# Performance work log

Hardware: AMD Instinct MI355X
Metric: run time of the kernel (lower is better)

Reference implementation:

```python
import jax, jax.numpy as jnp
import numpy as np

R_CUTOFF = 5.0
BASIS = 8
NMAX = 8
NSPECIES = 3
EMBED = 16


def _chebyshev_basis(r, r_cutoff, basis_size):
    fc = jnp.where(r < r_cutoff, 0.5 * jnp.cos(jnp.pi * r / r_cutoff) + 0.5, 0.0)
    x = 2.0 * (r / r_cutoff) ** 2 - 1.0
    polys = [jnp.ones_like(x), x]
    for n in range(2, basis_size):
        polys.append(2.0 * x * polys[-1] - polys[-2])
    basis = jnp.stack(polys[:basis_size], axis=-1)  # [E, basis]
    return 0.5 * (basis + 1.0) * fc[:, None]


def setup_inputs() -> dict:
    key = jax.random.key(0)
    ks = jax.random.split(key, 12)
    N, K = 20000, 32
    E = N * K
    positions = jax.random.normal(ks[0], (N, 3), dtype=jnp.float32)
    species = jax.random.randint(ks[1], (N,), 0, NSPECIES, dtype=jnp.int32)
    magmoms = jax.random.normal(ks[2], (N, 3), dtype=jnp.float32)
    # i-major edge list: exactly K edges per atom, grouped by center atom.
    i_idx = jnp.repeat(jnp.arange(N, dtype=jnp.int32), K)
    j_idx = jax.random.randint(ks[3], (E,), 0, N, dtype=jnp.int32)
    edge_index = jnp.stack([i_idx, j_idx], axis=0)
    shifts = jnp.zeros((E, 3), dtype=jnp.float32)
    rb_coefficients = 0.1 * jax.random.normal(ks[4], (NSPECIES * NSPECIES, NMAX, BASIS), dtype=jnp.float32)
    species_embedding = 0.1 * jax.random.normal(ks[5], (NSPECIES, EMBED), dtype=jnp.float32)
    struct_dim = NMAX + NMAX * (NMAX + 1)  # 80
    mag_dim = 3 + 7 * NMAX + 3 * NMAX * NMAX  # 251
    return {
        'positions': positions, 'species': species, 'magmoms': magmoms,
        'edge_index': edge_index, 'shifts': shifts,
        'rb_coefficients': rb_coefficients, 'species_embedding': species_embedding,
        'struct_shift': jnp.zeros(struct_dim, jnp.float32),
        'struct_scale': jnp.ones(struct_dim, jnp.float32),
        'mag_shift': jnp.zeros(mag_dim, jnp.float32),
        'mag_scale': jnp.ones(mag_dim, jnp.float32),
        'atomic_energy_shift': 0.1 * jax.random.normal(ks[6], (NSPECIES,), dtype=jnp.float32),
        'w_struct': 0.05 * jax.random.normal(ks[7], (EMBED + struct_dim,), dtype=jnp.float32),
        'b_struct': 0.05 * jax.random.normal(ks[8], (1,), dtype=jnp.float32),
        'w_mag': 0.05 * jax.random.normal(ks[9], (EMBED + mag_dim,), dtype=jnp.float32),
        'b_mag': 0.05 * jax.random.normal(ks[10], (1,), dtype=jnp.float32),
    }


def _forward(positions, magmoms, shifts, rb_coefficients, species_embedding,
             struct_shift, struct_scale, mag_shift, mag_scale, atomic_energy_shift,
             w_struct, b_struct, w_mag, b_mag, species, edge_index):
    N = positions.shape[0]
    E = edge_index.shape[1]
    K = E // N  # regular neighbor count (edge list is i-major)
    i_idx, j_idx = edge_index[0], edge_index[1]
    r_ij = positions[j_idx] - positions[i_idx] + shifts          # [E,3]
    dist = jnp.linalg.norm(r_ij, axis=-1)                        # [E]
    f_k = _chebyshev_basis(dist, R_CUTOFF, BASIS)                # [E,basis]
    pair_idx = species[i_idx] * NSPECIES + species[j_idx]
    phi = jnp.einsum('enk,ek->en', rb_coefficients[pair_idx], f_k)  # [E,n]
    seg = lambda x: jax.ops.segment_sum(x, i_idx, num_segments=N)
    d = jnp.maximum(dist, 1e-8)[:, None]
    r_hat = r_ij / d
    # --- structural descriptors ---
    d_radial = seg(phi)                                          # [N,n]
    P = seg(phi[:, :, None] * r_hat[:, None, :])                 # [N,n,3]
    PP = jnp.einsum('ina,ima->inm', P, P)
    tu = np.triu_indices(NMAX)
    d_ang_l1 = PP[:, tu[0], tu[1]]
    eye3 = jnp.eye(3, dtype=r_ij.dtype)
    traceless = r_hat[:, :, None] * r_hat[:, None, :] - eye3 / 3.0  # [E,3,3]
    Q = seg(phi[:, :, None, None] * traceless[:, None, :, :])       # [N,n,3,3]
    Qf = Q.reshape(N, NMAX, 9)
    QQ = jnp.einsum('ina,ima->inm', Qf, Qf)
    d_ang_l2 = QQ[:, tu[0], tu[1]]
    desc_struct = jnp.concatenate([d_radial, d_ang_l1, d_ang_l2], axis=-1)
    # --- magnetic descriptors ---
    u = jnp.sum(magmoms * magmoms, axis=-1)                      # [N]
    m_norm = jnp.linalg.norm(magmoms, axis=-1, keepdims=True)
    m_dir = jnp.where(m_norm > 1e-8, magmoms / jnp.maximum(m_norm, 1e-8), 0.0)
    M = seg(phi[:, :, None] * m_dir[j_idx][:, None, :])          # [N,n,3]
    # A_{nm}(i) = sum_{a<b within atom i's edge block} phi_n(a) phi_m(b) (r_a x r_b)
    phi_g = phi.reshape(N, K, NMAX)
    r_g = r_ij.reshape(N, K, 3)
    cross = jnp.cross(r_g[:, :, None, :], r_g[:, None, :, :])    # [N,K,K,3]
    mask = jnp.triu(jnp.ones((K, K), dtype=phi.dtype), k=1)
    tmp = jnp.einsum('iabd,ab,ibm->iamd', cross, mask, phi_g)    # [N,K,3,n]
    A = jnp.einsum('ian,iamd->inmd', phi_g, tmp)                 # [N,n,n,3]
    d_amp = jnp.stack([u, u ** 2, u ** 3], axis=-1)
    d_iso = jnp.sum(m_dir[:, None, :] * M, axis=-1)              # [N,n]
    Qm = jnp.einsum('anij,aj->ani', Q, m_dir)
    d_sia = jnp.sum(m_dir[:, None, :] * Qm, axis=-1)
    mQ = jnp.einsum('ai,amij->amj', m_dir, Q)
    d_sae = jnp.einsum('amj,anj->amn', mQ, M).reshape(N, -1)
    m_cross_M = jnp.cross(jnp.broadcast_to(m_dir[:, None, :], M.shape), M)
    d_dmi = jnp.einsum('inmd,imd->inm', A, m_cross_M).reshape(N, -1)
    u_col = u[:, None]
    d_amp_mix = jnp.concatenate([u_col * d_iso, u_col * d_sia, u_col * d_dmi], axis=-1)
    u_j = u[j_idx]
    d_nbr_amp = seg(phi * u_j[:, None])
    W = seg(phi[:, :, None] * (u_j[:, None] * m_dir[j_idx])[:, None, :])
    d_nbr_amp_ex = jnp.sum(m_dir[:, None, :] * W, axis=-1)
    d_nbr_amp_ex_mix = u_col * d_nbr_amp_ex
    desc_mag = jnp.concatenate([d_amp, d_iso, d_sia, d_sae, d_dmi, d_amp_mix,
                                d_nbr_amp, d_nbr_amp_ex, d_nbr_amp_ex_mix], axis=-1)
    # --- scaling + linear readout heads + per-species shift ---
    ds = (desc_struct - struct_shift) / struct_scale
    dm = (desc_mag - mag_shift) / mag_scale
    emb = species_embedding[species]
    e_struct = jnp.concatenate([emb, ds], axis=-1) @ w_struct + b_struct[0]
    e_mag = jnp.concatenate([emb, dm], axis=-1) @ w_mag + b_mag[0]
    return e_struct + e_mag + atomic_energy_shift[species]        # [N]


def reference(positions, species, magmoms, edge_index, shifts, rb_coefficients,
              species_embedding, struct_shift, struct_scale, mag_shift, mag_scale,
              atomic_energy_shift, w_struct, b_struct, w_mag, b_mag):
    return _forward(positions, magmoms, shifts, rb_coefficients, species_embedding,
                    struct_shift, struct_scale, mag_shift, mag_scale, atomic_energy_shift,
                    w_struct, b_struct, w_mag, b_mag, species, edge_index)
```

## Files before the change

kernel.cpp:

```cpp
#include <hip/hip_runtime.h>

#define NSPEC  3
#define EMBEDD 16
#define KMAX   32
#define RCUT   5.0f
#define PADR   36

__constant__ int TUN[36] = {0,0,0,0,0,0,0,0, 1,1,1,1,1,1,1, 2,2,2,2,2,2, 3,3,3,3,3, 4,4,4,4, 5,5,5, 6,6, 7};
__constant__ int TUM[36] = {0,1,2,3,4,5,6,7, 1,2,3,4,5,6,7, 2,3,4,5,6,7, 3,4,5,6,7, 4,5,6,7, 5,6,7, 6,7, 7};


template<int CTRL, int RMASK, bool BC>
__device__ __forceinline__ float dpp_mov0(float x) {
    return __int_as_float(__builtin_amdgcn_update_dpp(
        0, __float_as_int(x), CTRL, RMASK, 0xF, BC));
}
__device__ __forceinline__ float prefix32(float x) {
    x += dpp_mov0<0x111, 0xF, true >(x);
    x += dpp_mov0<0x112, 0xF, true >(x);
    x += dpp_mov0<0x114, 0xF, true >(x);
    x += dpp_mov0<0x118, 0xF, true >(x);
    x += dpp_mov0<0x142, 0xA, false>(x);
    return x;
}
__device__ __forceinline__ float swz_xor16(float x) {
    return __int_as_float(__builtin_amdgcn_ds_swizzle(__float_as_int(x), 0x401F));
}
__device__ __forceinline__ float red_k4(float x) {
    x += dpp_mov0<0x128, 0xF, true>(x);
    x += swz_xor16(x);
    return x;
}
__device__ __forceinline__ float red32(float x) {
    x += dpp_mov0<0x121, 0xF, true>(x);
    x += dpp_mov0<0x122, 0xF, true>(x);
    x += dpp_mov0<0x124, 0xF, true>(x);
    x += dpp_mov0<0x128, 0xF, true>(x);
    x += swz_xor16(x);
    return x;
}

__device__ __forceinline__ void lds_fence() {
    asm volatile("s_waitcnt lgkmcnt(0)" ::: "memory");
}

struct __align__(16) AtomLds {
    float phiT[8 * PADR];
    float rhx[KMAX], rhy[KMAX], rhz[KMAX];
    float mdx[KMAX], mdy[KMAX], mdz[KMAX];
    float uj[KMAX];
    float P4[8*4];
    float Q8[8*8];
    float M4[8*4];
    float mQ4[8*4];
    float wv4[8*4];
};

__global__ __launch_bounds__(256)
void magpot_setup(const float* __restrict__ sshift, const float* __restrict__ sscale,
                  const float* __restrict__ mshift, const float* __restrict__ mscale,
                  const float* __restrict__ wstruct, const float* __restrict__ bstruct,
                  const float* __restrict__ wmag, const float* __restrict__ bmag,
                  float* __restrict__ ws)
{
    __shared__ float red[4];
    const int t = threadIdx.x;
    float c = 0.0f;
    for (int idx = t; idx < 80; idx += 256) {
        const float w = wstruct[16 + idx] / sscale[idx];
        ws[idx] = w;
        c += w * sshift[idx];
    }
    for (int idx = t; idx < 251; idx += 256) {
        const float w = wmag[16 + idx] / mscale[idx];
        ws[80 + idx] = w;
        c += w * mshift[idx];
    }
    if (t < EMBEDD) ws[332 + t] = wstruct[t] + wmag[t];
    if (t < 64) {
        const int n = t >> 3, m = t & 7;
        ws[400 + m*8 + n] = wmag[16 + 83 + t]  / mscale[83 + t];
        ws[464 + m*8 + n] = wmag[16 + 163 + t] / mscale[163 + t];
    }
    #pragma unroll
    for (int d = 1; d <= 32; d <<= 1) c += __shfl_xor(c, d, 64);
    if ((t & 63) == 0) red[t >> 6] = c;
    __syncthreads();
    if (t == 0) ws[331] = bstruct[0] + bmag[0] - (red[0] + red[1] + red[2] + red[3]);
}

__global__ __launch_bounds__(256)
void magpot_main(const float* __restrict__ pos,
                 const int*   __restrict__ species,
                 const float* __restrict__ mag,
                 const int*   __restrict__ eidx,
                 const float* __restrict__ shifts,
                 const float* __restrict__ rb,
                 const float* __restrict__ semb,
                 const float* __restrict__ aes,
                 const float* __restrict__ ws,
                 float* __restrict__ out,
                 int N, int E, int K)
{
    __shared__ AtomLds lds[8];

    const int lane64 = threadIdx.x & 63;
    const int wv     = threadIdx.x >> 6;
    const int h      = lane64 >> 5;
    const int s      = lane64 & 31;
    const int ea     = 31 - s;
    const int i      = blockIdx.x * 8 + wv * 2 + h;
    const bool valid = (i < N);
    const int isafe  = valid ? i : 0;
    AtomLds& L = lds[wv * 2 + h];

    const float* wm = ws + 80;

    const float pix = pos[3*isafe+0], piy = pos[3*isafe+1], piz = pos[3*isafe+2];
    const int   spi = species[isafe];
    const float mgx = mag[3*isafe+0], mgy = mag[3*isafe+1], mgz = mag[3*isafe+2];
    const float u_i = mgx*mgx + mgy*mgy + mgz*mgz;
    const float mn_i = sqrtf(u_i);
    const float mi_inv = (mn_i > 1e-8f) ? (1.0f / mn_i) : 0.0f;
    const float mix = mgx*mi_inv, miy = mgy*mi_inv, miz = mgz*mi_inv;

    float phi[8];
    float rx = 0.0f, ry = 0.0f, rz = 0.0f;
    #pragma unroll
    for (int n = 0; n < 8; ++n) phi[n] = 0.0f;

    if (ea < K) {
        const int e = isafe * K + ea;
        const int j = eidx[E + e];
        rx = pos[3*j+0] - pix + shifts[3*e+0];
        ry = pos[3*j+1] - piy + shifts[3*e+1];
        rz = pos[3*j+2] - piz + shifts[3*e+2];
        const float dist = sqrtf(rx*rx + ry*ry + rz*rz);
        const float fc = (dist < RCUT)
            ? (0.5f * __builtin_amdgcn_cosf(dist * 0.1f) + 0.5f)
            : 0.0f;
        const float xr = dist * (1.0f/RCUT);
        const float x  = 2.0f * xr * xr - 1.0f;
        float f[8];
        {
            float Tm2 = 1.0f, Tm1 = x;
            f[0] = 0.5f * (Tm2 + 1.0f) * fc;
            f[1] = 0.5f * (Tm1 + 1.0f) * fc;
            #pragma unroll
            for (int k = 2; k < 8; ++k) {
                const float T = 2.0f * x * Tm1 - Tm2;
                Tm2 = Tm1; Tm1 = T;
                f[k] = 0.5f * (T + 1.0f) * fc;
            }
        }
        const int spj = species[j];
        const float4* rb4 = (const float4*)(rb + (spi * NSPEC + spj) * 64);
        #pragma unroll
        for (int n = 0; n < 8; ++n) {
            const float4 r0 = rb4[n*2+0];
            const float4 r1 = rb4[n*2+1];
            const float ph = r0.x*f[0] + r0.y*f[1] + r0.z*f[2] + r0.w*f[3]
                           + r1.x*f[4] + r1.y*f[5] + r1.z*f[6] + r1.w*f[7];
            phi[n] = ph;
            L.phiT[n*PADR + ea] = ph;
        }
        const float dinv = 1.0f / fmaxf(dist, 1e-8f);
        L.rhx[ea] = rx * dinv;
        L.rhy[ea] = ry * dinv;
        L.rhz[ea] = rz * dinv;
        const float mjx = mag[3*j+0], mjy = mag[3*j+1], mjz = mag[3*j+2];
        const float uj = mjx*mjx + mjy*mjy + mjz*mjz;
        const float mnj = sqrtf(uj);
        const float mjinv = (mnj > 1e-8f) ? (1.0f / mnj) : 0.0f;
        L.mdx[ea] = mjx * mjinv;
        L.mdy[ea] = mjy * mjinv;
        L.mdz[ea] = mjz * mjinv;
        L.uj[ea] = uj;
    } else {
        #pragma unroll
        for (int n = 0; n < 8; ++n) L.phiT[n*PADR + ea] = 0.0f;
        L.rhx[ea] = 0.0f; L.rhy[ea] = 0.0f; L.rhz[ea] = 0.0f;
        L.mdx[ea] = 0.0f; L.mdy[ea] = 0.0f; L.mdz[ea] = 0.0f;
        L.uj[ea] = 0.0f;
    }
    lds_fence();

    float p = 0.0f;

    {
        const int k4 = s >> 3;
        const int n  = s & 7;
        const float4* phR = (const float4*)&L.phiT[n*PADR + k4*8];
        const float4* hxR = (const float4*)&L.rhx[k4*8];
        const float4* hyR = (const float4*)&L.rhy[k4*8];
        const float4* hzR = (const float4*)&L.rhz[k4*8];
        const float4* dxR = (const float4*)&L.mdx[k4*8];
        const float4* dyR = (const float4*)&L.mdy[k4*8];
        const float4* dzR = (const float4*)&L.mdz[k4*8];
        const float4* ujR = (const float4*)&L.uj[k4*8];

        float a_dr = 0.0f;
        float aP0 = 0.0f, aP1 = 0.0f, aP2 = 0.0f;
        float aQ0 = 0.0f, aQ1 = 0.0f, aQ2 = 0.0f, aQ3 = 0.0f, aQ4 = 0.0f, aQ5 = 0.0f;
        float aM0 = 0.0f, aM1 = 0.0f, aM2 = 0.0f;
        float a_nb = 0.0f;
        float aW0 = 0.0f, aW1 = 0.0f, aW2 = 0.0f;

        auto acc = [&](float ph, float hx, float hy, float hz,
                       float dx, float dy, float dz, float uj) {
            a_dr += ph;
            aP0 += ph*hx; aP1 += ph*hy; aP2 += ph*hz;
            aQ0 += ph*(hx*hx - (1.0f/3.0f));
            aQ1 += ph*(hx*hy);
            aQ2 += ph*(hx*hz);
            aQ3 += ph*(hy*hy - (1.0f/3.0f));
            aQ4 += ph*(hy*hz);
            aQ5 += ph*(hz*hz - (1.0f/3.0f));
            aM0 += ph*dx; aM1 += ph*dy; aM2 += ph*dz;
            const float pu = ph*uj;
            a_nb += pu;
            aW0 += pu*dx; aW1 += pu*dy; aW2 += pu*dz;
        };
        #pragma unroll
        for (int q = 0; q < 2; ++q) {
            const float4 ph4 = phR[q], hx4 = hxR[q], hy4 = hyR[q], hz4 = hzR[q];
            const float4 dx4 = dxR[q], dy4 = dyR[q], dz4 = dzR[q], uj4 = ujR[q];
            acc(ph4.x, hx4.x, hy4.x, hz4.x, dx4.x, dy4.x, dz4.x, uj4.x);
            acc(ph4.y, hx4.y, hy4.y, hz4.y, dx4.y, dy4.y, dz4.y, uj4.y);
            acc(ph4.z, hx4.z, hy4.z, hz4.z, dx4.z, dy4.z, dz4.z, uj4.z);
            acc(ph4.w, hx4.w, hy4.w, hz4.w, dx4.w, dy4.w, dz4.w, uj4.w);
        }
        a_dr = red_k4(a_dr);
        aP0 = red_k4(aP0); aP1 = red_k4(aP1); aP2 = red_k4(aP2);
        aQ0 = red_k4(aQ0); aQ1 = red_k4(aQ1); aQ2 = red_k4(aQ2);
        aQ3 = red_k4(aQ3); aQ4 = red_k4(aQ4); aQ5 = red_k4(aQ5);
        aM0 = red_k4(aM0); aM1 = red_k4(aM1); aM2 = red_k4(aM2);
        a_nb = red_k4(a_nb);
        aW0 = red_k4(aW0); aW1 = red_k4(aW1); aW2 = red_k4(aW2);

        if (k4 == 0) {
            ((float4*)L.P4)[n]      = make_float4(aP0, aP1, aP2, 0.0f);
            ((float4*)L.Q8)[2*n]    = make_float4(aQ0, aQ1, aQ2, aQ3);
            ((float4*)L.Q8)[2*n+1]  = make_float4(aQ4, aQ5, 0.0f, 0.0f);
            ((float4*)L.M4)[n]      = make_float4(aM0, aM1, aM2, 0.0f);
            const float mq0 = aQ0*mix + aQ1*miy + aQ2*miz;
            const float mq1 = aQ1*mix + aQ3*miy + aQ4*miz;
            const float mq2 = aQ2*mix + aQ4*miy + aQ5*miz;
            ((float4*)L.mQ4)[n]     = make_float4(mq0, mq1, mq2, 0.0f);
            ((float4*)L.wv4)[n]     = make_float4(miy*aM2 - miz*aM1,
                                                  miz*aM0 - mix*aM2,
                                                  mix*aM1 - miy*aM0, 0.0f);
            const float diso = mix*aM0 + miy*aM1 + miz*aM2;
            const float dsia = aQ0*mix*mix + aQ3*miy*miy + aQ5*miz*miz
                             + 2.0f*(aQ1*mix*miy + aQ2*mix*miz + aQ4*miy*miz);
            const float dnex = mix*aW0 + miy*aW1 + miz*aW2;
            p += a_dr * ws[n] + a_nb * wm[227 + n]
               + diso * wm[3 + n]  + dsia * wm[11 + n]  + dnex * wm[235 + n]
               + u_i * (diso * wm[147 + n] + dsia * wm[155 + n] + dnex * wm[243 + n]);
        }
        if (s == 8) {
            const float u2 = u_i * u_i;
            p += u_i * wm[0] + u2 * wm[1] + u2 * u_i * wm[2];
        }
        if (s < EMBEDD)
            p += semb[spi * EMBEDD + s] * ws[332 + s];
    }
    lds_fence();

    {
        float B[8];
        #pragma unroll
        for (int m = 0; m < 8; ++m) {
            float a1 = 0.0f, a2 = 0.0f;
            #pragma unroll
            for (int n = 0; n < 8; ++n) {
                a1 = fmaf(phi[n], ws[400 + m*8 + n], a1);
                a2 = fmaf(phi[n], ws[464 + m*8 + n], a2);
            }
            B[m] = a1 + u_i * a2;
        }
        float cdmi = 0.0f;
        #pragma unroll
        for (int m = 0; m < 8; ++m) {
            const float4 wvm = ((const float4*)L.wv4)[m];
            const float vx = phi[m] * rx;
            const float vy = phi[m] * ry;
            const float vz = phi[m] * rz;
            const float Sx = prefix32(vx) - vx;
            const float Sy = prefix32(vy) - vy;
            const float Sz = prefix32(vz) - vz;
            const float cx = ry*Sz - rz*Sy;
            const float cy = rz*Sx - rx*Sz;
            const float cz = rx*Sy - ry*Sx;
            cdmi = fmaf(B[m], cx*wvm.x + cy*wvm.y + cz*wvm.z, cdmi);
        }
        p += cdmi;
    }

    {
        #pragma unroll
        for (int t2 = 0; t2 < 2; ++t2) {
            const int idx = s + t2*32;
            const int m4 = idx >> 3, n4 = idx & 7;
            const float4 mQm = ((const float4*)L.mQ4)[m4];
            const float4 Mn  = ((const float4*)L.M4)[n4];
            p += (mQm.x*Mn.x + mQm.y*Mn.y + mQm.z*Mn.z) * wm[19 + idx];
        }
        #pragma unroll
        for (int t2 = 0; t2 < 2; ++t2) {
            const int idx = s + t2*32;
            if (idx < 36) {
                const int a = TUN[idx], b = TUM[idx];
                const float4 Pa = ((const float4*)L.P4)[a];
                const float4 Pb = ((const float4*)L.P4)[b];
                const float pp = Pa.x*Pb.x + Pa.y*Pb.y + Pa.z*Pb.z;
                const float4 Qa0 = ((const float4*)L.Q8)[2*a], Qa1 = ((const float4*)L.Q8)[2*a+1];
                const float4 Qb0 = ((const float4*)L.Q8)[2*b], Qb1 = ((const float4*)L.Q8)[2*b+1];
                const float qq = Qa0.x*Qb0.x + Qa0.w*Qb0.w + Qa1.y*Qb1.y
                       + 2.0f*(Qa0.y*Qb0.y + Qa0.z*Qb0.z + Qa1.x*Qb1.x);
                p += pp * ws[8 + idx] + qq * ws[44 + idx];
            }
        }
    }

    p = red32(p);
    if (s == 0 && valid)
        out[i] = p + ws[331] + aes[spi];
}

extern "C" void kernel_launch(void* const* d_in, const int* in_sizes, int n_in,
                              void* d_out, int out_size, void* d_ws, size_t ws_size,
                              hipStream_t stream) {
    const float* pos     = (const float*)d_in[0];
    const int*   spc     = (const int*)  d_in[1];
    const float* mg      = (const float*)d_in[2];
    const int*   eidx    = (const int*)  d_in[3];
    const float* shf     = (const float*)d_in[4];
    const float* rb      = (const float*)d_in[5];
    const float* semb    = (const float*)d_in[6];
    const float* sshift  = (const float*)d_in[7];
    const float* sscale  = (const float*)d_in[8];
    const float* mshift  = (const float*)d_in[9];
    const float* mscale  = (const float*)d_in[10];
    const float* aes     = (const float*)d_in[11];
    const float* wstruct = (const float*)d_in[12];
    const float* bstruct = (const float*)d_in[13];
    const float* wmag    = (const float*)d_in[14];
    const float* bmag    = (const float*)d_in[15];
    float* out = (float*)d_out;
    float* ws  = (float*)d_ws;

    const int N = in_sizes[1];
    const int E = in_sizes[3] / 2;
    const int K = E / N;

    hipLaunchKernelGGL(magpot_setup, dim3(1), dim3(256), 0, stream,
                       sshift, sscale, mshift, mscale, wstruct, bstruct, wmag, bmag, ws);
    hipLaunchKernelGGL(magpot_main, dim3((N + 7) / 8), dim3(256), 0, stream,
                       pos, spc, mg, eidx, shf, rb, semb, aes, ws, out, N, E, K);
}
```

Before: 123.7 us.

## Split per-edge feature computation into separate kernel staged through global workspace

Moves the per-edge radial basis, direction and neighbour-moment computation into a new edge-parallel kernel that writes features to a global workspace. The setup work is folded into that kernel as an extra block. The per-atom kernel now reads these features from global memory instead of computing them and staging them through LDS. This trades an extra round trip of roughly 16 floats per edge through HBM/L2 for better parallelism and a simpler main kernel, and it removes the LDS arrays. The per-atom accumulation now issues strided global loads per lane, where before it read vectorised LDS data.

```diff
diff --git a/kernel.cpp b/kernel.cpp
--- a/kernel.cpp
+++ b/kernel.cpp
@@ -4,7 +4,6 @@
 #define EMBEDD 16
 #define KMAX   32
 #define RCUT   5.0f
-#define PADR   36
 
 __constant__ int TUN[36] = {0,0,0,0,0,0,0,0, 1,1,1,1,1,1,1, 2,2,2,2,2,2, 3,3,3,3,3, 4,4,4,4, 5,5,5, 6,6, 7};
 __constant__ int TUM[36] = {0,1,2,3,4,5,6,7, 1,2,3,4,5,6,7, 2,3,4,5,6,7, 3,4,5,6,7, 4,5,6,7, 5,6,7, 6,7, 7};
@@ -39,29 +38,15 @@
     x += swz_xor16(x);
     return x;
 }
-
 __device__ __forceinline__ void lds_fence() {
     asm volatile("s_waitcnt lgkmcnt(0)" ::: "memory");
 }
 
-struct __align__(16) AtomLds {
-    float phiT[8 * PADR];
-    float rhx[KMAX], rhy[KMAX], rhz[KMAX];
-    float mdx[KMAX], mdy[KMAX], mdz[KMAX];
-    float uj[KMAX];
-    float P4[8*4];
-    float Q8[8*8];
-    float M4[8*4];
-    float mQ4[8*4];
-    float wv4[8*4];
-};
-
-__global__ __launch_bounds__(256)
-void magpot_setup(const float* __restrict__ sshift, const float* __restrict__ sscale,
-                  const float* __restrict__ mshift, const float* __restrict__ mscale,
-                  const float* __restrict__ wstruct, const float* __restrict__ bstruct,
-                  const float* __restrict__ wmag, const float* __restrict__ bmag,
-                  float* __restrict__ ws)
+__device__ void do_setup(const float* sshift, const float* sscale,
+                         const float* mshift, const float* mscale,
+                         const float* wstruct, const float* bstruct,
+                         const float* wmag, const float* bmag,
+                         float* ws)
 {
     __shared__ float red[4];
     const int t = threadIdx.x;
@@ -90,12 +75,90 @@
 }
 
 __global__ __launch_bounds__(256)
-void magpot_main(const float* __restrict__ pos,
-                 const int*   __restrict__ species,
+void magpot_edges(const float* __restrict__ pos,
+                  const int*   __restrict__ species,
+                  const float* __restrict__ mag,
+                  const int*   __restrict__ eidx,
+                  const float* __restrict__ shifts,
+                  const float* __restrict__ rb,
+                  const float* __restrict__ sshift, const float* __restrict__ sscale,
+                  const float* __restrict__ mshift, const float* __restrict__ mscale,
+                  const float* __restrict__ wstruct, const float* __restrict__ bstruct,
+                  const float* __restrict__ wmag, const float* __restrict__ bmag,
+                  float* __restrict__ ws,
+                  int E, int nEdgeBlocks)
+{
+    if ((int)blockIdx.x == nEdgeBlocks) {
+        do_setup(sshift, sscale, mshift, mscale, wstruct, bstruct, wmag, bmag, ws);
+        return;
+    }
+    const int e = blockIdx.x * 256 + threadIdx.x;
+    if (e >= E) return;
+
+    const int i = eidx[e];
+    const int j = eidx[E + e];
+    const float rx = pos[3*j+0] - pos[3*i+0] + shifts[3*e+0];
+    const float ry = pos[3*j+1] - pos[3*i+1] + shifts[3*e+1];
+    const float rz = pos[3*j+2] - pos[3*i+2] + shifts[3*e+2];
+    const float dist = sqrtf(rx*rx + ry*ry + rz*rz);
+    const float fc = (dist < RCUT)
+        ? (0.5f * __builtin_amdgcn_cosf(dist * 0.1f) + 0.5f)
+        : 0.0f;
+    const float xr = dist * (1.0f/RCUT);
+    const float x  = 2.0f * xr * xr - 1.0f;
+    float f[8];
+    {
+        float Tm2 = 1.0f, Tm1 = x;
+        f[0] = 0.5f * (Tm2 + 1.0f) * fc;
+        f[1] = 0.5f * (Tm1 + 1.0f) * fc;
+        #pragma unroll
+        for (int k = 2; k < 8; ++k) {
+            const float T = 2.0f * x * Tm1 - Tm2;
+            Tm2 = Tm1; Tm1 = T;
+            f[k] = 0.5f * (T + 1.0f) * fc;
+        }
+    }
+    const int pair = species[i] * NSPEC + species[j];
+    const float4* rb4 = (const float4*)(rb + pair * 64);
+    float4 ph0, ph1;
+    {
+        float phv[8];
+        #pragma unroll
+        for (int n = 0; n < 8; ++n) {
+            const float4 r0 = rb4[n*2+0];
+            const float4 r1 = rb4[n*2+1];
+            phv[n] = r0.x*f[0] + r0.y*f[1] + r0.z*f[2] + r0.w*f[3]
+                   + r1.x*f[4] + r1.y*f[5] + r1.z*f[6] + r1.w*f[7];
+        }
+        ph0 = make_float4(phv[0], phv[1], phv[2], phv[3]);
+        ph1 = make_float4(phv[4], phv[5], phv[6], phv[7]);
+    }
+    const float dinv = 1.0f / fmaxf(dist, 1e-8f);
+    const float mjx = mag[3*j+0], mjy = mag[3*j+1], mjz = mag[3*j+2];
+    const float uj = mjx*mjx + mjy*mjy + mjz*mjz;
+    const float mnj = sqrtf(uj);
+    const float mjinv = (mnj > 1e-8f) ? (1.0f / mnj) : 0.0f;
+
+    float4* phi8 = (float4*)(ws + 1024);
+    float4* r4g  = (float4*)(ws + 1024 + 8*(size_t)E);
+    float4* md4g = (float4*)(ws + 1024 + 12*(size_t)E);
+    phi8[2*e]   = ph0;
+    phi8[2*e+1] = ph1;
+    r4g[e]  = make_float4(rx*dinv, ry*dinv, rz*dinv, dist);
+    md4g[e] = make_float4(mjx*mjinv, mjy*mjinv, mjz*mjinv, uj);
+}
+
+struct __align__(16) AtomLds {
+    float P4[32];
+    float Q8[64];
+    float M4[32];
+    float mQ4[32];
+    float wv4[32];
+};
+
+__global__ __launch_bounds__(256)
+void magpot_main(const int*   __restrict__ species,
                  const float* __restrict__ mag,
-                 const int*   __restrict__ eidx,
-                 const float* __restrict__ shifts,
-                 const float* __restrict__ rb,
                  const float* __restrict__ semb,
                  const float* __restrict__ aes,
                  const float* __restrict__ ws,
@@ -115,8 +178,11 @@
     AtomLds& L = lds[wv * 2 + h];
 
     const float* wm = ws + 80;
-
-    const float pix = pos[3*isafe+0], piy = pos[3*isafe+1], piz = pos[3*isafe+2];
+    const float*  phig  = ws + 1024;
+    const float4* phi8g = (const float4*)(ws + 1024);
+    const float4* r4g   = (const float4*)(ws + 1024 + 8*(size_t)E);
+    const float4* md4g  = (const float4*)(ws + 1024 + 12*(size_t)E);
+
     const int   spi = species[isafe];
     const float mgx = mag[3*isafe+0], mgy = mag[3*isafe+1], mgz = mag[3*isafe+2];
     const float u_i = mgx*mgx + mgy*mgy + mgz*mgz;
@@ -128,76 +194,21 @@
     float rx = 0.0f, ry = 0.0f, rz = 0.0f;
     #pragma unroll
     for (int n = 0; n < 8; ++n) phi[n] = 0.0f;
-
     if (ea < K) {
         const int e = isafe * K + ea;
-        const int j = eidx[E + e];
-        rx = pos[3*j+0] - pix + shifts[3*e+0];
-        ry = pos[3*j+1] - piy + shifts[3*e+1];
-        rz = pos[3*j+2] - piz + shifts[3*e+2];
-        const float dist = sqrtf(rx*rx + ry*ry + rz*rz);
-        const float fc = (dist < RCUT)
-            ? (0.5f * __builtin_amdgcn_cosf(dist * 0.1f) + 0.5f)
-            : 0.0f;
-        const float xr = dist * (1.0f/RCUT);
-        const float x  = 2.0f * xr * xr - 1.0f;
-        float f[8];
-        {
-            float Tm2 = 1.0f, Tm1 = x;
-            f[0] = 0.5f * (Tm2 + 1.0f) * fc;
-            f[1] = 0.5f * (Tm1 + 1.0f) * fc;
-            #pragma unroll
-            for (int k = 2; k < 8; ++k) {
-                const float T = 2.0f * x * Tm1 - Tm2;
-                Tm2 = Tm1; Tm1 = T;
-                f[k] = 0.5f * (T + 1.0f) * fc;
-            }
-        }
-        const int spj = species[j];
-        const float4* rb4 = (const float4*)(rb + (spi * NSPEC + spj) * 64);
-        #pragma unroll
-        for (int n = 0; n < 8; ++n) {
-            const float4 r0 = rb4[n*2+0];
-            const float4 r1 = rb4[n*2+1];
-            const float ph = r0.x*f[0] + r0.y*f[1] + r0.z*f[2] + r0.w*f[3]
-                           + r1.x*f[4] + r1.y*f[5] + r1.z*f[6] + r1.w*f[7];
-            phi[n] = ph;
-            L.phiT[n*PADR + ea] = ph;
-        }
-        const float dinv = 1.0f / fmaxf(dist, 1e-8f);
-        L.rhx[ea] = rx * dinv;
-        L.rhy[ea] = ry * dinv;
-        L.rhz[ea] = rz * dinv;
-        const float mjx = mag[3*j+0], mjy = mag[3*j+1], mjz = mag[3*j+2];
-        const float uj = mjx*mjx + mjy*mjy + mjz*mjz;
-        const float mnj = sqrtf(uj);
-        const float mjinv = (mnj > 1e-8f) ? (1.0f / mnj) : 0.0f;
-        L.mdx[ea] = mjx * mjinv;
-        L.mdy[ea] = mjy * mjinv;
-        L.mdz[ea] = mjz * mjinv;
-        L.uj[ea] = uj;
-    } else {
-        #pragma unroll
-        for (int n = 0; n < 8; ++n) L.phiT[n*PADR + ea] = 0.0f;
-        L.rhx[ea] = 0.0f; L.rhy[ea] = 0.0f; L.rhz[ea] = 0.0f;
-        L.mdx[ea] = 0.0f; L.mdy[ea] = 0.0f; L.mdz[ea] = 0.0f;
-        L.uj[ea] = 0.0f;
-    }
-    lds_fence();
+        const float4 p0 = phi8g[2*e], p1 = phi8g[2*e+1];
+        phi[0]=p0.x; phi[1]=p0.y; phi[2]=p0.z; phi[3]=p0.w;
+        phi[4]=p1.x; phi[5]=p1.y; phi[6]=p1.z; phi[7]=p1.w;
+        const float4 rv = r4g[e];
+        rx = rv.x * rv.w; ry = rv.y * rv.w; rz = rv.z * rv.w;
+    }
 
     float p = 0.0f;
 
     {
         const int k4 = s >> 3;
         const int n  = s & 7;
-        const float4* phR = (const float4*)&L.phiT[n*PADR + k4*8];
-        const float4* hxR = (const float4*)&L.rhx[k4*8];
-        const float4* hyR = (const float4*)&L.rhy[k4*8];
-        const float4* hzR = (const float4*)&L.rhz[k4*8];
-        const float4* dxR = (const float4*)&L.mdx[k4*8];
-        const float4* dyR = (const float4*)&L.mdy[k4*8];
-        const float4* dzR = (const float4*)&L.mdz[k4*8];
-        const float4* ujR = (const float4*)&L.uj[k4*8];
+        const int base = isafe * K + k4*8;
 
         float a_dr = 0.0f;
         float aP0 = 0.0f, aP1 = 0.0f, aP2 = 0.0f;
@@ -206,8 +217,15 @@
         float a_nb = 0.0f;
         float aW0 = 0.0f, aW1 = 0.0f, aW2 = 0.0f;
 
-        auto acc = [&](float ph, float hx, float hy, float hz,
-                       float dx, float dy, float dz, float uj) {
+        #pragma unroll
+        for (int q = 0; q < 8; ++q) {
+            const bool ok = (k4*8 + q) < K;
+            const int ee = ok ? (base + q) : (isafe * K);
+            float ph = phig[(size_t)ee*8 + n];
+            ph = ok ? ph : 0.0f;
+            const float4 rv = r4g[ee];
+            const float4 mv = md4g[ee];
+            const float hx = rv.x, hy = rv.y, hz = rv.z;
             a_dr += ph;
             aP0 += ph*hx; aP1 += ph*hy; aP2 += ph*hz;
             aQ0 += ph*(hx*hx - (1.0f/3.0f));
@@ -216,19 +234,10 @@
             aQ3 += ph*(hy*hy - (1.0f/3.0f));
             aQ4 += ph*(hy*hz);
             aQ5 += ph*(hz*hz - (1.0f/3.0f));
-            aM0 += ph*dx; aM1 += ph*dy; aM2 += ph*dz;
-            const float pu = ph*uj;
+            aM0 += ph*mv.x; aM1 += ph*mv.y; aM2 += ph*mv.z;
+            const float pu = ph*mv.w;
             a_nb += pu;
-            aW0 += pu*dx; aW1 += pu*dy; aW2 += pu*dz;
-        };
-        #pragma unroll
-        for (int q = 0; q < 2; ++q) {
-            const float4 ph4 = phR[q], hx4 = hxR[q], hy4 = hyR[q], hz4 = hzR[q];
-            const float4 dx4 = dxR[q], dy4 = dyR[q], dz4 = dzR[q], uj4 = ujR[q];
-            acc(ph4.x, hx4.x, hy4.x, hz4.x, dx4.x, dy4.x, dz4.x, uj4.x);
-            acc(ph4.y, hx4.y, hy4.y, hz4.y, dx4.y, dy4.y, dz4.y, uj4.y);
-            acc(ph4.z, hx4.z, hy4.z, hz4.z, dx4.z, dy4.z, dz4.z, uj4.z);
-            acc(ph4.w, hx4.w, hy4.w, hz4.w, dx4.w, dy4.w, dz4.w, uj4.w);
+            aW0 += pu*mv.x; aW1 += pu*mv.y; aW2 += pu*mv.z;
         }
         a_dr = red_k4(a_dr);
         aP0 = red_k4(aP0); aP1 = red_k4(aP1); aP2 = red_k4(aP2);
@@ -239,17 +248,17 @@
         aW0 = red_k4(aW0); aW1 = red_k4(aW1); aW2 = red_k4(aW2);
 
         if (k4 == 0) {
-            ((float4*)L.P4)[n]      = make_float4(aP0, aP1, aP2, 0.0f);
-            ((float4*)L.Q8)[2*n]    = make_float4(aQ0, aQ1, aQ2, aQ3);
-            ((float4*)L.Q8)[2*n+1]  = make_float4(aQ4, aQ5, 0.0f, 0.0f);
-            ((float4*)L.M4)[n]      = make_float4(aM0, aM1, aM2, 0.0f);
+            ((float4*)L.P4)[n]     = make_float4(aP0, aP1, aP2, 0.0f);
+            ((float4*)L.Q8)[2*n]   = make_float4(aQ0, aQ1, aQ2, aQ3);
+            ((float4*)L.Q8)[2*n+1] = make_float4(aQ4, aQ5, 0.0f, 0.0f);
+            ((float4*)L.M4)[n]     = make_float4(aM0, aM1, aM2, 0.0f);
             const float mq0 = aQ0*mix + aQ1*miy + aQ2*miz;
             const float mq1 = aQ1*mix + aQ3*miy + aQ4*miz;
             const float mq2 = aQ2*mix + aQ4*miy + aQ5*miz;
-            ((float4*)L.mQ4)[n]     = make_float4(mq0, mq1, mq2, 0.0f);
-            ((float4*)L.wv4)[n]     = make_float4(miy*aM2 - miz*aM1,
-                                                  miz*aM0 - mix*aM2,
-                                                  mix*aM1 - miy*aM0, 0.0f);
+            ((float4*)L.mQ4)[n]    = make_float4(mq0, mq1, mq2, 0.0f);
+            ((float4*)L.wv4)[n]    = make_float4(miy*aM2 - miz*aM1,
+                                                 miz*aM0 - mix*aM2,
+                                                 mix*aM1 - miy*aM0, 0.0f);
             const float diso = mix*aM0 + miy*aM1 + miz*aM2;
             const float dsia = aQ0*mix*mix + aQ3*miy*miy + aQ5*miz*miz
                              + 2.0f*(aQ1*mix*miy + aQ2*mix*miz + aQ4*miy*miz);
@@ -354,8 +363,11 @@
     const int E = in_sizes[3] / 2;
     const int K = E / N;
 
-    hipLaunchKernelGGL(magpot_setup, dim3(1), dim3(256), 0, stream,
-                       sshift, sscale, mshift, mscale, wstruct, bstruct, wmag, bmag, ws);
+    const int nEdgeBlocks = (E + 255) / 256;
+    hipLaunchKernelGGL(magpot_edges, dim3(nEdgeBlocks + 1), dim3(256), 0, stream,
+                       pos, spc, mg, eidx, shf, rb,
+                       sshift, sscale, mshift, mscale, wstruct, bstruct, wmag, bmag,
+                       ws, E, nEdgeBlocks);
     hipLaunchKernelGGL(magpot_main, dim3((N + 7) / 8), dim3(256), 0, stream,
-                       pos, spc, mg, eidx, shf, rb, semb, aes, ws, out, N, E, K);
-}
+                       spc, mg, semb, aes, ws, out, N, E, K);
+}
```

Result: slower. 137.2 us (+10.9%).
